# Kernel optimization log

Hardware: AMD Instinct MI355X
Metric: run time of the kernel (lower is better)

Reference implementation:

```python
import jax, jax.numpy as jnp
import numpy as np

B, F, D = 4096, 32, 32
LAYER_SIZE = [128, 128]


def setup_inputs() -> dict:
    key = jax.random.key(0)
    k1, k2, k3 = jax.random.split(key, 3)
    inputs = jax.random.normal(k1, (B, F, D), dtype=jnp.float32)
    # CIN filters: shape [1, field_nums[0]*field_nums[i], field_nums[i+1]]
    field_nums = [F] + LAYER_SIZE
    filter_0 = (jax.random.normal(k2, (1, field_nums[0] * field_nums[0], field_nums[1]), dtype=jnp.float32) * 0.05)
    filter_1 = (jax.random.normal(k3, (1, field_nums[0] * field_nums[1], field_nums[2]), dtype=jnp.float32) * 0.05)
    return {"inputs": inputs, "filter_0": filter_0, "filter_1": filter_1}


def _cin_forward(inputs, filters):
    x0 = inputs          # [B, F, D] -- hidden_nn_layers[0]
    prev = inputs        # hidden_nn_layers[-1]
    outs = []
    for W in filters:    # W: [1, F*M, N]
        # outer product over field dims: [B, F, M, D]
        z = jnp.einsum('bhd,bmd->bhmd', x0, prev)
        b, h, m, d = z.shape
        z = z.reshape(b, h * m, d)                 # [B, F*M, D]
        # 1x1 conv over the F*M axis == contraction with W[0]: [F*M, N]
        cur = jnp.einsum('bpd,pn->bnd', z, W[0])   # [B, N, D]
        cur = jax.nn.relu(cur)
        prev = cur
        outs.append(cur)
    result = jnp.concatenate(outs, axis=1)         # [B, sum(layer_size), D]
    return jnp.sum(result, axis=-1)                # [B, sum(layer_size)]


def reference(inputs, filter_0, filter_1):
    return _cin_forward(inputs, (filter_0, filter_1))
```

## Files before the change

### kernel.cpp

```cpp
#include <hip/hip_runtime.h>


typedef _Float16 half_t;
typedef _Float16 half4v __attribute__((ext_vector_type(4)));
typedef _Float16 half8 __attribute__((ext_vector_type(8)));
typedef float f32x16 __attribute__((ext_vector_type(16)));

__global__ void prep_w_kernel(const float* __restrict__ W0,
                              const float* __restrict__ W1,
                              half_t* __restrict__ Wp0,
                              half_t* __restrict__ Wp1) {
  int gid = blockIdx.x * 256 + threadIdx.x;
  int n = gid & 127;
  int tg = (gid >> 7) & 1;
  int s = gid >> 8;
  const float* W;
  half_t* Wp;
  int M, sl;
  if (s < 64) { W = W0; Wp = Wp0; M = 32; sl = s; }
  else        { W = W1; Wp = Wp1; M = 128; sl = s - 64; }
  int h = sl & 31, mc = sl >> 5;
  int kbase = h * M + mc * 16 + tg * 8;
  half8 v;
#pragma unroll
  for (int j = 0; j < 8; ++j) v[j] = (half_t)W[(size_t)(kbase + j) * 128 + n];
  *(half8*)(Wp + ((size_t)(sl * 2 + tg) * 128 + n) * 8) = v;
}

__device__ __forceinline__ int pswz(int row, int m) {
  return row * 128 + (((m >> 3) ^ (row & 15)) << 3) + (m & 7);
}

__device__ __forceinline__ f32x16 mfma3216(half8 a, half8 b, f32x16 c) {
  return __builtin_amdgcn_mfma_f32_32x32x16_f16(a, b, c, 0, 0, 0);
}

template <int MC, bool L1>
__device__ __forceinline__ void layer_loop(const half_t* __restrict__ Wp,
                                           const half_t* __restrict__ psrc,
                                           const half_t* __restrict__ xrd,
                                           int woff, int l31, int hi,
                                           f32x16 acc[4]) {
  half8 B0a = *(const half8*)(Wp + 0 * 2048 + woff);
  half8 B1a = *(const half8*)(Wp + 1 * 2048 + woff);
  half8 B0b = *(const half8*)(Wp + 2 * 2048 + woff);
  half8 B1b = *(const half8*)(Wp + 3 * 2048 + woff);
  half8 xqa = *(const half8*)(xrd);
  half8 xqb = *(const half8*)(xrd + 256);

  half8 P[4];
#pragma unroll
  for (int rt = 0; rt < 4; ++rt)
    P[rt] = L1 ? *(const half8*)&psrc[(rt * 32 + l31) * 40 + hi * 8]
               : *(const half8*)&psrc[pswz(rt * 32 + l31, hi * 8)];

#pragma unroll 1
  for (int mc = 0; mc < MC; ++mc) {
#pragma unroll 1
    for (int p = 0; p < 8; ++p) {
      const int g0 = mc * 16 + 2 * p;
#pragma unroll
      for (int rt = 0; rt < 4; ++rt)
        acc[rt] = mfma3216(P[rt] * xqa[rt * 2 + 0], B0a, acc[rt]);
#pragma unroll
      for (int rt = 0; rt < 4; ++rt)
        acc[rt] = mfma3216(P[rt] * xqa[rt * 2 + 1], B1a, acc[rt]);
      {
        const int sn = (2 * (g0 + 2)) & (MC * 32 - 1);
        B0a = *(const half8*)(Wp + (size_t)sn * 2048 + woff);
        B1a = *(const half8*)(Wp + (size_t)(sn + 1) * 2048 + woff);
        xqa = *(const half8*)(xrd + ((2 * p + 2) & 15) * 256);
      }
#pragma unroll
      for (int rt = 0; rt < 4; ++rt)
        acc[rt] = mfma3216(P[rt] * xqb[rt * 2 + 0], B0b, acc[rt]);
#pragma unroll
      for (int rt = 0; rt < 4; ++rt)
        acc[rt] = mfma3216(P[rt] * xqb[rt * 2 + 1], B1b, acc[rt]);
      {
        const int sn = (2 * (g0 + 3)) & (MC * 32 - 1);
        B0b = *(const half8*)(Wp + (size_t)sn * 2048 + woff);
        B1b = *(const half8*)(Wp + (size_t)(sn + 1) * 2048 + woff);
        xqb = *(const half8*)(xrd + ((2 * p + 3) & 15) * 256);
      }
    }
    if (mc + 1 < MC) {
      const int mn = (mc + 1) * 16;
#pragma unroll
      for (int rt = 0; rt < 4; ++rt)
        P[rt] = L1 ? *(const half8*)&psrc[(rt * 32 + l31) * 40 + mn + hi * 8]
                   : *(const half8*)&psrc[pswz(rt * 32 + l31, mn + hi * 8)];
    }
  }
}

__global__ __launch_bounds__(256, 4) void cin_fused_kernel(
    const float* __restrict__ x0,
    const half_t* __restrict__ Wp0,
    const half_t* __restrict__ Wp1,
    float* __restrict__ out) {
  __shared__ half_t xsf3[16 * 256];
  __shared__ half_t prevT[4 * 32 * 128];
  half_t* xT = prevT;

  const int tid = threadIdx.x;
  const int b0 = blockIdx.x * 4;

  const float4* x4 = (const float4*)(x0 + (size_t)b0 * 1024);
#pragma unroll
  for (int r = 0; r < 4; ++r) {
    int q = r * 256 + tid;
    float4 v = x4[q];
    int e = q * 4;
    int bi = e >> 10, h = (e >> 5) & 31, d0 = e & 31;
    half4v hv = {(half_t)v.x, (half_t)v.y, (half_t)v.z, (half_t)v.w};
#pragma unroll
    for (int j = 0; j < 4; ++j) {
      xsf3[(h >> 1) * 256 + (d0 + j) * 8 + bi * 2 + (h & 1)] = hv[j];
      xT[(bi * 32 + d0 + j) * 40 + h] = hv[j];
    }
  }
  __syncthreads();

  const int lane = tid & 63;
  const int l31 = lane & 31;
  const int hi = lane >> 5;
  const int wave = tid >> 6;
  const int n0 = wave * 32;

  const int woff = hi * 1024 + (n0 + l31) * 8;
  const half_t* xrd = &xsf3[l31 * 8];

  f32x16 acc[4];
#pragma unroll
  for (int rt = 0; rt < 4; ++rt)
#pragma unroll
    for (int r = 0; r < 16; ++r) acc[rt][r] = 0.f;

  layer_loop<2, true>(Wp0, xT, xrd, woff, l31, hi, acc);

  __syncthreads();

#pragma unroll
  for (int rt = 0; rt < 4; ++rt) {
    float s = 0.f;
#pragma unroll
    for (int r = 0; r < 16; ++r) {
      float v = acc[rt][r];
      v = v > 0.f ? v : 0.f;
      s += v;
      int d = (r & 3) + ((r >> 2) << 3) + hi * 4;
      prevT[pswz(rt * 32 + d, n0 + l31)] = (half_t)v;
      acc[rt][r] = 0.f;
    }
    s += __shfl_down(s, 32);
    if (lane < 32) out[(size_t)(b0 + rt) * 256 + n0 + lane] = s;
  }
  __syncthreads();

  layer_loop<8, false>(Wp1, prevT, xrd, woff, l31, hi, acc);

#pragma unroll
  for (int rt = 0; rt < 4; ++rt) {
    float s = 0.f;
#pragma unroll
    for (int r = 0; r < 16; ++r) {
      float v = acc[rt][r];
      s += v > 0.f ? v : 0.f;
    }
    s += __shfl_down(s, 32);
    if (lane < 32) out[(size_t)(b0 + rt) * 256 + 128 + n0 + lane] = s;
  }
}

extern "C" void kernel_launch(void* const* d_in, const int* in_sizes, int n_in,
                              void* d_out, int out_size, void* d_ws,
                              size_t ws_size, hipStream_t stream) {
  const float* x0 = (const float*)d_in[0];
  const float* w0 = (const float*)d_in[1];
  const float* w1 = (const float*)d_in[2];
  float* out = (float*)d_out;
  char* ws = (char*)d_ws;

  half_t* Wp0 = (half_t*)(ws);
  half_t* Wp1 = (half_t*)(ws + 64 * 2048 * 2);

  hipLaunchKernelGGL(prep_w_kernel, dim3(320), dim3(256), 0, stream, w0, w1,
                     Wp0, Wp1);
  hipLaunchKernelGGL(cin_fused_kernel, dim3(1024), dim3(256), 0, stream, x0,
                     Wp0, Wp1, out);
}
```

Measured before the change: 211.3 us.

## Process eight batches per block with 2x2 wave tiling and dual column tiles

Doubles batch rows per block and splits waves into a 2x2 grid over batch quads and output-channel halves, each wave computing two 32-column tiles. Each elementwise-scaled A fragment is reused across two MFMAs and per-batch weight traffic is halved. In exchange, accumulator registers double, launch bounds drop to 2 waves per SIMD, LDS usage grows, and the grid halves to 512 blocks, reducing occupancy and latency hiding.

```diff
diff --git a/kernel.cpp b/kernel.cpp
--- a/kernel.cpp
+++ b/kernel.cpp
@@ -38,21 +38,25 @@
 template <int MC, bool L1>
 __device__ __forceinline__ void layer_loop(const half_t* __restrict__ Wp,
                                            const half_t* __restrict__ psrc,
-                                           const half_t* __restrict__ xrd,
-                                           int woff, int l31, int hi,
-                                           f32x16 acc[4]) {
-  half8 B0a = *(const half8*)(Wp + 0 * 2048 + woff);
-  half8 B1a = *(const half8*)(Wp + 1 * 2048 + woff);
-  half8 B0b = *(const half8*)(Wp + 2 * 2048 + woff);
-  half8 B1b = *(const half8*)(Wp + 3 * 2048 + woff);
-  half8 xqa = *(const half8*)(xrd);
-  half8 xqb = *(const half8*)(xrd + 256);
+                                           const half_t* __restrict__ xQw,
+                                           int woff0, int woff1, int rowb,
+                                           int l31, int hi, f32x16 acc[4][2]) {
+  half8 B0a0 = *(const half8*)(Wp + 0 * 2048 + woff0);
+  half8 B0a1 = *(const half8*)(Wp + 0 * 2048 + woff1);
+  half8 B1a0 = *(const half8*)(Wp + 1 * 2048 + woff0);
+  half8 B1a1 = *(const half8*)(Wp + 1 * 2048 + woff1);
+  half8 B0b0 = *(const half8*)(Wp + 2 * 2048 + woff0);
+  half8 B0b1 = *(const half8*)(Wp + 2 * 2048 + woff1);
+  half8 B1b0 = *(const half8*)(Wp + 3 * 2048 + woff0);
+  half8 B1b1 = *(const half8*)(Wp + 3 * 2048 + woff1);
+  half8 xqa = *(const half8*)(xQw);
+  half8 xqb = *(const half8*)(xQw + 256);
 
   half8 P[4];
 #pragma unroll
   for (int rt = 0; rt < 4; ++rt)
-    P[rt] = L1 ? *(const half8*)&psrc[(rt * 32 + l31) * 40 + hi * 8]
-               : *(const half8*)&psrc[pswz(rt * 32 + l31, hi * 8)];
+    P[rt] = L1 ? *(const half8*)&psrc[(rowb + rt * 32 + l31) * 40 + hi * 8]
+               : *(const half8*)&psrc[pswz(rowb + rt * 32 + l31, hi * 8)];
 
 #pragma unroll 1
   for (int mc = 0; mc < MC; ++mc) {
@@ -60,63 +64,83 @@
     for (int p = 0; p < 8; ++p) {
       const int g0 = mc * 16 + 2 * p;
 #pragma unroll
-      for (int rt = 0; rt < 4; ++rt)
-        acc[rt] = mfma3216(P[rt] * xqa[rt * 2 + 0], B0a, acc[rt]);
-#pragma unroll
-      for (int rt = 0; rt < 4; ++rt)
-        acc[rt] = mfma3216(P[rt] * xqa[rt * 2 + 1], B1a, acc[rt]);
+      for (int rt = 0; rt < 4; ++rt) {
+        half8 Af = P[rt] * xqa[rt * 2 + 0];
+        acc[rt][0] = mfma3216(Af, B0a0, acc[rt][0]);
+        acc[rt][1] = mfma3216(Af, B0a1, acc[rt][1]);
+      }
+#pragma unroll
+      for (int rt = 0; rt < 4; ++rt) {
+        half8 Af = P[rt] * xqa[rt * 2 + 1];
+        acc[rt][0] = mfma3216(Af, B1a0, acc[rt][0]);
+        acc[rt][1] = mfma3216(Af, B1a1, acc[rt][1]);
+      }
       {
         const int sn = (2 * (g0 + 2)) & (MC * 32 - 1);
-        B0a = *(const half8*)(Wp + (size_t)sn * 2048 + woff);
-        B1a = *(const half8*)(Wp + (size_t)(sn + 1) * 2048 + woff);
-        xqa = *(const half8*)(xrd + ((2 * p + 2) & 15) * 256);
-      }
-#pragma unroll
-      for (int rt = 0; rt < 4; ++rt)
-        acc[rt] = mfma3216(P[rt] * xqb[rt * 2 + 0], B0b, acc[rt]);
-#pragma unroll
-      for (int rt = 0; rt < 4; ++rt)
-        acc[rt] = mfma3216(P[rt] * xqb[rt * 2 + 1], B1b, acc[rt]);
+        B0a0 = *(const half8*)(Wp + (size_t)sn * 2048 + woff0);
+        B0a1 = *(const half8*)(Wp + (size_t)sn * 2048 + woff1);
+        B1a0 = *(const half8*)(Wp + (size_t)(sn + 1) * 2048 + woff0);
+        B1a1 = *(const half8*)(Wp + (size_t)(sn + 1) * 2048 + woff1);
+        xqa = *(const half8*)(xQw + ((2 * p + 2) & 15) * 256);
+      }
+#pragma unroll
+      for (int rt = 0; rt < 4; ++rt) {
+        half8 Af = P[rt] * xqb[rt * 2 + 0];
+        acc[rt][0] = mfma3216(Af, B0b0, acc[rt][0]);
+        acc[rt][1] = mfma3216(Af, B0b1, acc[rt][1]);
+      }
+#pragma unroll
+      for (int rt = 0; rt < 4; ++rt) {
+        half8 Af = P[rt] * xqb[rt * 2 + 1];
+        acc[rt][0] = mfma3216(Af, B1b0, acc[rt][0]);
+        acc[rt][1] = mfma3216(Af, B1b1, acc[rt][1]);
+      }
       {
         const int sn = (2 * (g0 + 3)) & (MC * 32 - 1);
-        B0b = *(const half8*)(Wp + (size_t)sn * 2048 + woff);
-        B1b = *(const half8*)(Wp + (size_t)(sn + 1) * 2048 + woff);
-        xqb = *(const half8*)(xrd + ((2 * p + 3) & 15) * 256);
+        B0b0 = *(const half8*)(Wp + (size_t)sn * 2048 + woff0);
+        B0b1 = *(const half8*)(Wp + (size_t)sn * 2048 + woff1);
+        B1b0 = *(const half8*)(Wp + (size_t)(sn + 1) * 2048 + woff0);
+        B1b1 = *(const half8*)(Wp + (size_t)(sn + 1) * 2048 + woff1);
+        xqb = *(const half8*)(xQw + ((2 * p + 3) & 15) * 256);
       }
     }
     if (mc + 1 < MC) {
       const int mn = (mc + 1) * 16;
 #pragma unroll
       for (int rt = 0; rt < 4; ++rt)
-        P[rt] = L1 ? *(const half8*)&psrc[(rt * 32 + l31) * 40 + mn + hi * 8]
-                   : *(const half8*)&psrc[pswz(rt * 32 + l31, mn + hi * 8)];
-    }
-  }
-}
-
-__global__ __launch_bounds__(256, 4) void cin_fused_kernel(
+        P[rt] = L1 ? *(const half8*)&psrc[(rowb + rt * 32 + l31) * 40 + mn +
+                                          hi * 8]
+                   : *(const half8*)&psrc[pswz(rowb + rt * 32 + l31,
+                                               mn + hi * 8)];
+    }
+  }
+}
+
+__global__ __launch_bounds__(256, 2) void cin_fused_kernel(
     const float* __restrict__ x0,
     const half_t* __restrict__ Wp0,
     const half_t* __restrict__ Wp1,
     float* __restrict__ out) {
-  __shared__ half_t xsf3[16 * 256];
-  __shared__ half_t prevT[4 * 32 * 128];
+  __shared__ half_t xQ[2 * 16 * 32 * 8];
+  __shared__ half_t prevT[8 * 32 * 128];
   half_t* xT = prevT;
 
   const int tid = threadIdx.x;
-  const int b0 = blockIdx.x * 4;
+  const int b0 = blockIdx.x * 8;
 
   const float4* x4 = (const float4*)(x0 + (size_t)b0 * 1024);
 #pragma unroll
-  for (int r = 0; r < 4; ++r) {
+  for (int r = 0; r < 8; ++r) {
     int q = r * 256 + tid;
     float4 v = x4[q];
-    int e = q * 4;
-    int bi = e >> 10, h = (e >> 5) & 31, d0 = e & 31;
+    int e4 = q * 4;
+    int bi = e4 >> 10, h = (e4 >> 5) & 31, d0 = e4 & 31;
     half4v hv = {(half_t)v.x, (half_t)v.y, (half_t)v.z, (half_t)v.w};
+    const int quad = bi >> 2, rtl = bi & 3;
 #pragma unroll
     for (int j = 0; j < 4; ++j) {
-      xsf3[(h >> 1) * 256 + (d0 + j) * 8 + bi * 2 + (h & 1)] = hv[j];
+      xQ[quad * 4096 + (h >> 1) * 256 + (d0 + j) * 8 + rtl * 2 + (h & 1)] =
+          hv[j];
       xT[(bi * 32 + d0 + j) * 40 + h] = hv[j];
     }
   }
@@ -126,50 +150,64 @@
   const int l31 = lane & 31;
   const int hi = lane >> 5;
   const int wave = tid >> 6;
-  const int n0 = wave * 32;
-
-  const int woff = hi * 1024 + (n0 + l31) * 8;
-  const half_t* xrd = &xsf3[l31 * 8];
-
-  f32x16 acc[4];
+  const int wr = wave >> 1;
+  const int wc = wave & 1;
+
+  const int woff0 = hi * 1024 + (wc * 64 + l31) * 8;
+  const int woff1 = hi * 1024 + (wc * 64 + 32 + l31) * 8;
+  const int rowb = wr * 128;
+  const half_t* xQw = xQ + wr * 4096 + l31 * 8;
+
+  f32x16 acc[4][2];
 #pragma unroll
   for (int rt = 0; rt < 4; ++rt)
 #pragma unroll
-    for (int r = 0; r < 16; ++r) acc[rt][r] = 0.f;
-
-  layer_loop<2, true>(Wp0, xT, xrd, woff, l31, hi, acc);
+    for (int ct = 0; ct < 2; ++ct)
+#pragma unroll
+      for (int r = 0; r < 16; ++r) acc[rt][ct][r] = 0.f;
+
+  layer_loop<2, true>(Wp0, xT, xQw, woff0, woff1, rowb, l31, hi, acc);
 
   __syncthreads();
 
 #pragma unroll
   for (int rt = 0; rt < 4; ++rt) {
-    float s = 0.f;
-#pragma unroll
-    for (int r = 0; r < 16; ++r) {
-      float v = acc[rt][r];
-      v = v > 0.f ? v : 0.f;
-      s += v;
-      int d = (r & 3) + ((r >> 2) << 3) + hi * 4;
-      prevT[pswz(rt * 32 + d, n0 + l31)] = (half_t)v;
-      acc[rt][r] = 0.f;
-    }
-    s += __shfl_down(s, 32);
-    if (lane < 32) out[(size_t)(b0 + rt) * 256 + n0 + lane] = s;
+#pragma unroll
+    for (int ct = 0; ct < 2; ++ct) {
+      float s = 0.f;
+#pragma unroll
+      for (int r = 0; r < 16; ++r) {
+        float v = acc[rt][ct][r];
+        v = v > 0.f ? v : 0.f;
+        s += v;
+        int d = (r & 3) + ((r >> 2) << 3) + hi * 4;
+        prevT[pswz(rowb + rt * 32 + d, wc * 64 + ct * 32 + l31)] = (half_t)v;
+        acc[rt][ct][r] = 0.f;
+      }
+      s += __shfl_down(s, 32);
+      if (lane < 32)
+        out[(size_t)(b0 + wr * 4 + rt) * 256 + wc * 64 + ct * 32 + lane] = s;
+    }
   }
   __syncthreads();
 
-  layer_loop<8, false>(Wp1, prevT, xrd, woff, l31, hi, acc);
+  layer_loop<8, false>(Wp1, prevT, xQw, woff0, woff1, rowb, l31, hi, acc);
 
 #pragma unroll
   for (int rt = 0; rt < 4; ++rt) {
-    float s = 0.f;
-#pragma unroll
-    for (int r = 0; r < 16; ++r) {
-      float v = acc[rt][r];
-      s += v > 0.f ? v : 0.f;
-    }
-    s += __shfl_down(s, 32);
-    if (lane < 32) out[(size_t)(b0 + rt) * 256 + 128 + n0 + lane] = s;
+#pragma unroll
+    for (int ct = 0; ct < 2; ++ct) {
+      float s = 0.f;
+#pragma unroll
+      for (int r = 0; r < 16; ++r) {
+        float v = acc[rt][ct][r];
+        s += v > 0.f ? v : 0.f;
+      }
+      s += __shfl_down(s, 32);
+      if (lane < 32)
+        out[(size_t)(b0 + wr * 4 + rt) * 256 + 128 + wc * 64 + ct * 32 +
+            lane] = s;
+    }
   }
 }
 
@@ -187,6 +225,6 @@
 
   hipLaunchKernelGGL(prep_w_kernel, dim3(320), dim3(256), 0, stream, w0, w1,
                      Wp0, Wp1);
-  hipLaunchKernelGGL(cin_fused_kernel, dim3(1024), dim3(256), 0, stream, x0,
+  hipLaunchKernelGGL(cin_fused_kernel, dim3(512), dim3(256), 0, stream, x0,
                      Wp0, Wp1, out);
 }
```

New measurement: 191.8 us. -9.2%, faster.
